# Optimization experiments

Hardware: AMD Instinct MI355X
Metric: run time of the kernel (lower is better)

## Reference

```python
import jax, jax.numpy as jnp
from jax import lax
import numpy as np

DN = ('NCHW', 'OIHW', 'NCHW')
DL = 64
B = 1024


def _cbr(x, w, g, b, stride, pad):
    """Conv2d(bias=False) -> BatchNorm2d (training stats, eps=1e-5) -> ReLU."""
    y = lax.conv_general_dilated(x, w, (stride, stride), [(pad, pad), (pad, pad)],
                                 dimension_numbers=DN)
    m = y.mean(axis=(0, 2, 3), keepdims=True)
    v = ((y - m) ** 2).mean(axis=(0, 2, 3), keepdims=True)  # biased var, as torch BN
    y = (y - m) * lax.rsqrt(v + 1e-5)
    return jax.nn.relu(y * g[None, :, None, None] + b[None, :, None, None])


def setup_inputs() -> dict:
    key = jax.random.key(0)
    ks = jax.random.split(key, 7)
    dl = DL
    inp = {
        'x': jax.random.normal(ks[0], (B, 3, 32, 32), jnp.float32),
        'w1': jax.random.normal(ks[1], (32, 3, 3, 3), jnp.float32) * 0.1,
        'w2': jax.random.normal(ks[2], (64, 32, 3, 3), jnp.float32) * 0.05,
        'w3': jax.random.normal(ks[3], (64, 64, 3, 3), jnp.float32) * 0.05,
        'wa': jax.random.normal(ks[4], (dl, 32, 1, 1), jnp.float32) * 0.1,
        'ws1': jax.random.normal(ks[5], (3 * dl, 32, 3, 3), jnp.float32) * 0.05,
        'ws2': jax.random.normal(ks[6], (3 * dl, 3 * dl, 3, 3), jnp.float32) * 0.03,
    }
    for i, c in enumerate([32, 64, 64, dl, 3 * dl, 3 * dl]):
        inp[f'g{i}'] = jnp.ones((c,), jnp.float32)
        inp[f'b{i}'] = jnp.zeros((c,), jnp.float32)
    return inp


def _encoder(x, w1, w2, w3, wa, ws1, ws2,
             g0, b0, g1, b1, g2, b2, g3, b3, g4, b4, g5, b5):
    dl = DL
    h = _cbr(x, w1, g0, b0, 1, 1)            # [B, 32, 32, 32]
    h = _cbr(h, w2, g1, b1, 1, 1)            # [B, 64, 32, 32]
    AS = _cbr(h, w3, g2, b2, 2, 1)           # [B, 64, 16, 16]
    A_, S_ = jnp.split(AS, 2, axis=1)        # each [B, 32, 16, 16]
    A = _cbr(A_, wa, g3, b3, 1, 0)           # [B, dl, 16, 16]
    S = _cbr(S_, ws1, g4, b4, 1, 1)          # [B, 3dl, 16, 16]
    S = _cbr(S, ws2, g5, b5, 2, 1)           # [B, 3dl, 8, 8]
    b, _, ps, _ = S.shape
    S = S.reshape(b, dl, 3, ps, ps)

    # per-sample conv_transpose2d(A[ii] [1,dl,pa,pa], weight S[ii] [dl,3,ps,ps],
    # stride=2, padding=3) expressed as lhs-dilated cross-correlation with
    # flipped, channel-swapped kernel; batched via vmap (no Python loop).
    pad = ps - 1 - 3  # k - 1 - torch_padding = 4

    def ct(a, s):  # a: [dl,16,16], s: [dl,3,8,8]
        wt = jnp.flip(s, (-2, -1)).transpose(1, 0, 2, 3)  # [3, dl, 8, 8]
        return lax.conv_general_dilated(a[None], wt, (1, 1),
                                        [(pad, pad), (pad, pad)],
                                        lhs_dilation=(2, 2),
                                        dimension_numbers=DN)[0]

    recon = jax.vmap(ct)(A, S)               # [B, 3, 32, 32]
    img = jax.nn.sigmoid(x)
    recon = jax.nn.sigmoid(recon)
    l1 = jnp.mean((img - recon) ** 2)
    l2 = jnp.mean(jax.nn.relu(S))
    logp = jax.nn.log_softmax(S, axis=1)     # softmax over dl axis (dim=1)
    l3 = -jnp.mean(jnp.exp(logp) * logp)
    return A, S, 0.1 * l1, 0.1 * l2, 0.1 * l3


def reference(x, w1, w2, w3, wa, ws1, ws2,
              g0, b0, g1, b1, g2, b2, g3, b3, g4, b4, g5, b5):
    return _encoder(x, w1, w2, w3, wa, ws1, ws2,
                    g0, b0, g1, b1, g2, b2, g3, b3, g4, b4, g5, b5)
```

## Files before the change

kernel.cpp:

```cpp
#include <hip/hip_runtime.h>
#include <math.h>


typedef __attribute__((ext_vector_type(8))) short short8v;
typedef __attribute__((ext_vector_type(4))) short short4v;
typedef __attribute__((ext_vector_type(4))) float f32x4;

__device__ __forceinline__ unsigned short f2bf(float f) {
  union { float f; unsigned u; } a; a.f = f;
  unsigned r = a.u + 0x7fffu + ((a.u >> 16) & 1u);
  return (unsigned short)(r >> 16);
}
__device__ __forceinline__ float bf2f(unsigned short h) {
  union { unsigned u; float f; } a; a.u = ((unsigned)h) << 16;
  return a.f;
}

__device__ __forceinline__ float wave_reduce(float v) {
#pragma unroll
  for (int off = 32; off; off >>= 1) v += __shfl_down(v, off, 64);
  return v;
}

template <int CI, int CO>
__device__ __forceinline__ void reord1(const float* __restrict__ w,
                                       unsigned short* __restrict__ wr,
                                       int idx) {
  int e = idx & 7;
  int t = idx >> 3;
  int co = t % CO; t /= CO;
  int ci8 = t % (CI / 8);
  int kk = t / (CI / 8);
  int ci = ci8 * 8 + e;
  wr[idx] = f2bf(w[((size_t)co * CI + ci) * 9 + kk]);
}

__global__ __launch_bounds__(256) void wreord_all_k(
    const float* __restrict__ w2, const float* __restrict__ w3,
    const float* __restrict__ ws1, const float* __restrict__ ws2,
    unsigned short* __restrict__ w2r, unsigned short* __restrict__ w3r,
    unsigned short* __restrict__ ws1r, unsigned short* __restrict__ ws2r) {
  int idx = blockIdx.x * 256 + threadIdx.x;
  if (idx < 18432) reord1<32, 64>(w2, w2r, idx);
  else if (idx < 55296) reord1<64, 64>(w3, w3r, idx - 18432);
  else if (idx < 110592) reord1<32, 192>(ws1, ws1r, idx - 55296);
  else if (idx < 442368) reord1<192, 192>(ws2, ws2r, idx - 110592);
}

__global__ __launch_bounds__(256) void conv0_k(const float* __restrict__ in,
                                               const float* __restrict__ w,
                                               unsigned short* __restrict__ outB,
                                               double* __restrict__ part) {
  __shared__ __align__(16) float tile[3][34][36];
  const int b = blockIdx.x;
  const int co0 = blockIdx.y * 8;
  const int tid = threadIdx.x;
  const int row = tid >> 3, x0 = (tid & 7) * 4;
  const int wv = tid >> 6;

  float* tf = &tile[0][0][0];
  for (int i = tid; i < 918; i += 256)
    *(float4*)(tf + i * 4) = make_float4(0.f, 0.f, 0.f, 0.f);
  __syncthreads();
  for (int i = tid; i < 768; i += 256) {
    int x4 = i & 7, yy = (i >> 3) & 31, c = i >> 8;
    float4 v = *(const float4*)&in[(((size_t)b * 3 + c) * 32 + yy) * 32 + x4 * 4];
    float* dst = &tile[c][yy + 1][1 + x4 * 4];
    dst[0] = v.x; dst[1] = v.y; dst[2] = v.z; dst[3] = v.w;
  }
  __syncthreads();

  float acc[4][8];
#pragma unroll
  for (int p = 0; p < 4; ++p)
#pragma unroll
    for (int co = 0; co < 8; ++co) acc[p][co] = 0.f;

#pragma unroll
  for (int c = 0; c < 3; ++c)
#pragma unroll
    for (int ky = 0; ky < 3; ++ky) {
      const float* tr = &tile[c][row + ky][x0];
      float4 vlo = *(const float4*)tr;
      float2 vhi = *(const float2*)(tr + 4);
      float v[6] = {vlo.x, vlo.y, vlo.z, vlo.w, vhi.x, vhi.y};
#pragma unroll
      for (int kx = 0; kx < 3; ++kx)
#pragma unroll
        for (int co = 0; co < 8; ++co) {
          float wvv = w[((size_t)(co0 + co) * 3 + c) * 9 + ky * 3 + kx];
#pragma unroll
          for (int p = 0; p < 4; ++p)
            acc[p][co] = fmaf(v[p + kx], wvv, acc[p][co]);
        }
    }
#pragma unroll
  for (int p = 0; p < 4; ++p) {
    short8v o;
#pragma unroll
    for (int co = 0; co < 8; ++co) o[co] = (short)f2bf(acc[p][co]);
    *(short8v*)&outB[(((size_t)b * 32 + row) * 32 + x0 + p) * 32 + co0] = o;
  }

  float s8[8], q8[8];
#pragma unroll
  for (int co = 0; co < 8; ++co) {
    float s = 0.f, q = 0.f;
#pragma unroll
    for (int p = 0; p < 4; ++p) {
      float v = acc[p][co];
      s += v;
      q = fmaf(v, v, q);
    }
    s8[co] = wave_reduce(s);
    q8[co] = wave_reduce(q);
  }
  __syncthreads();
  float* sb = (float*)tile;
  if ((tid & 63) == 0) {
#pragma unroll
    for (int co = 0; co < 8; ++co) {
      sb[wv * 8 + co] = s8[co];
      sb[32 + wv * 8 + co] = q8[co];
    }
  }
  __syncthreads();
  if (tid < 8) {
    float S = 0.f, Q = 0.f;
#pragma unroll
    for (int k = 0; k < 4; ++k) {
      S += sb[k * 8 + tid];
      Q += sb[32 + k * 8 + tid];
    }
    size_t slot = ((size_t)(co0 + tid) * 1024 + b) * 2;
    part[slot] = (double)S;
    part[slot + 1] = (double)Q;
  }
}

template <int CI_T, int CI0, int CI, int CIP, int CO, int COB, int IHW,
          int OHW, int STRIDE, int ORPB, int WM, int WN, int CTM, int CTN,
          bool OUT_BF16T>
__global__ __launch_bounds__(512) void convgemm_k(
    const unsigned short* __restrict__ inT, const float* __restrict__ ss,
    const unsigned short* __restrict__ wr_w, float* __restrict__ outF,
    unsigned short* __restrict__ outB, double* __restrict__ part) {
  constexpr int IR = (ORPB - 1) * STRIDE + 3;
  constexpr int IW2 = IHW + 2;
  constexpr int NPX = ORPB * OHW;
  constexpr int NPIX = OHW * OHW;
  constexpr bool SWZ = (STRIDE == 2);
  static_assert(WM * WN == 8, "8 waves");
  static_assert(WN * CTN * 16 == NPX, "px tiling");
  static_assert(WM * CTM * 16 == COB, "co tiling");
  static_assert((IR * IW2 * CIP) % 4 == 0, "zero fill");
  static_assert(IR * IW2 * CIP * 2 >= 8 * CTM * 16 * 2 * 4, "stats overlay");
  static_assert(!SWZ || (CI / 8) % 8 == 0, "swizzle octet closure");
  __shared__ __align__(16) unsigned short st[IR * IW2 * CIP];

  const int b = blockIdx.x;
  const int oy0 = blockIdx.y * ORPB;
  const int co_base = blockIdx.z * COB;
  const int tid = threadIdx.x;
  const int w = tid >> 6, l = tid & 63;
  const int l16 = l & 15, g = l >> 4;
  const int wrow = w / WN, wcol = w % WN;

  {
    uint2 z = make_uint2(0u, 0u);
    uint2* stz = (uint2*)st;
    constexpr int NZ = IR * IW2 * CIP / 4;
    for (int i = tid; i < NZ; i += 512) stz[i] = z;
  }
  __syncthreads();

  {
    constexpr int CPP = CI / 8;
    constexpr int NCH = IR * IHW * CPP;
    const int r0in = oy0 * STRIDE - 1;
    for (int i = tid; i < NCH; i += 512) {
      int c8 = i % CPP;
      int xx = (i / CPP) % IHW;
      int ir = i / (CPP * IHW);
      int iy = r0in + ir;
      if ((unsigned)iy < (unsigned)IHW) {
        short8v raw = *(const short8v*)&inT[(((size_t)b * IHW + iy) * IHW + xx) *
                                            CI_T + CI0 + c8 * 8];
        f32x4 sc0 = *(const f32x4*)&ss[CI0 + c8 * 8];
        f32x4 sc1 = *(const f32x4*)&ss[CI0 + c8 * 8 + 4];
        f32x4 sh0 = *(const f32x4*)&ss[CI_T + CI0 + c8 * 8];
        f32x4 sh1 = *(const f32x4*)&ss[CI_T + CI0 + c8 * 8 + 4];
        short4v lo, hi;
#pragma unroll
        for (int e = 0; e < 4; ++e) {
          float f = bf2f((unsigned short)raw[e]);
          f = fmaxf(fmaf(f, sc0[e], sh0[e]), 0.f);
          lo[e] = (short)f2bf(f);
        }
#pragma unroll
        for (int e = 0; e < 4; ++e) {
          float f = bf2f((unsigned short)raw[e + 4]);
          f = fmaxf(fmaf(f, sc1[e], sh1[e]), 0.f);
          hi[e] = (short)f2bf(f);
        }
        int xcol = xx + 1;
        int gran = SWZ ? (c8 ^ (xcol & 7)) : c8;
        int pp = SWZ ? ((xcol >> 1) & 1) : 0;
        unsigned short* dst = &st[(ir * IW2 + xcol) * CIP + gran * 8];
        *(short4v*)(dst + 4 * pp) = lo;
        *(short4v*)(dst + 4 * (1 - pp)) = hi;
      }
    }
  }
  __syncthreads();

  int prow[CTN], pxx[CTN];
#pragma unroll
  for (int pn = 0; pn < CTN; ++pn) {
    int pxl = (wcol * CTN + pn) * 16 + l16;
    int ly = pxl / OHW, lx = pxl % OHW;
    prow[pn] = (ly * STRIDE * IW2 + lx * STRIDE) * CIP;
    pxx[pn] = lx * STRIDE;
  }
  const int co_off = co_base + wrow * CTM * 16 + l16;

  f32x4 acc[CTM][CTN];
#pragma unroll
  for (int cm = 0; cm < CTM; ++cm)
#pragma unroll
    for (int pn = 0; pn < CTN; ++pn) {
      f32x4 z = {0.f, 0.f, 0.f, 0.f};
      acc[cm][pn] = z;
    }

#pragma unroll 3
  for (int kk = 0; kk < 9; ++kk) {
    const int ky = kk / 3, kx = kk % 3;
    const int rowadd = (ky * IW2 + kx) * CIP;
#pragma unroll
    for (int cs = 0; cs < CI / 32; ++cs) {
      short8v bfr[CTN];
#pragma unroll
      for (int pn = 0; pn < CTN; ++pn) {
        int col = pxx[pn] + kx;
        int gran = cs * 4 + g;
        int pp = 0;
        if (SWZ) {
          gran ^= (col & 7);
          pp = (col >> 1) & 1;
        }
        const unsigned short* bp = &st[prow[pn] + rowadd + gran * 8];
        short4v lo = *(const short4v*)(bp + 4 * pp);
        short4v hi = *(const short4v*)(bp + 4 * (1 - pp));
        short8v v = {lo[0], lo[1], lo[2], lo[3], hi[0], hi[1], hi[2], hi[3]};
        bfr[pn] = v;
      }
      const unsigned short* wb =
          wr_w + ((size_t)(kk * (CI / 8) + cs * 4 + g) * CO + co_off) * 8;
      short8v afr[CTM];
#pragma unroll
      for (int cm = 0; cm < CTM; ++cm)
        afr[cm] = *(const short8v*)(wb + cm * 128);
#pragma unroll
      for (int cm = 0; cm < CTM; ++cm)
#pragma unroll
        for (int pn = 0; pn < CTN; ++pn)
          acc[cm][pn] = __builtin_amdgcn_mfma_f32_16x16x32_bf16(
              afr[cm], bfr[pn], acc[cm][pn], 0, 0, 0);
    }
  }

#pragma unroll
  for (int cm = 0; cm < CTM; ++cm)
#pragma unroll
    for (int pn = 0; pn < CTN; ++pn) {
      int pxl = (wcol * CTN + pn) * 16 + l16;
      size_t pxg = (size_t)oy0 * OHW + pxl;
      int co = co_base + (wrow * CTM + cm) * 16 + g * 4;
      if (OUT_BF16T) {
        unsigned d0 = (unsigned)f2bf(acc[cm][pn][0]) |
                      ((unsigned)f2bf(acc[cm][pn][1]) << 16);
        unsigned d1 = (unsigned)f2bf(acc[cm][pn][2]) |
                      ((unsigned)f2bf(acc[cm][pn][3]) << 16);
        unsigned* dst = (unsigned*)&outB[((size_t)b * NPIX + pxg) * CO + co];
        dst[0] = d0;
        dst[1] = d1;
      } else {
#pragma unroll
        for (int r = 0; r < 4; ++r)
          outF[((size_t)b * CO + co + r) * NPIX + pxg] = acc[cm][pn][r];
      }
    }

  float sst[CTM][4], qst[CTM][4];
#pragma unroll
  for (int cm = 0; cm < CTM; ++cm)
#pragma unroll
    for (int r = 0; r < 4; ++r) {
      float s = 0.f, q = 0.f;
#pragma unroll
      for (int pn = 0; pn < CTN; ++pn) {
        float v = acc[cm][pn][r];
        s += v;
        q = fmaf(v, v, q);
      }
#pragma unroll
      for (int mask = 1; mask < 16; mask <<= 1) {
        s += __shfl_xor(s, mask, 64);
        q += __shfl_xor(q, mask, 64);
      }
      sst[cm][r] = s;
      qst[cm][r] = q;
    }
  __syncthreads();
  float* sbuf = (float*)st;
  float* qbuf = sbuf + 8 * CTM * 16;
  if (l16 == 0) {
#pragma unroll
    for (int cm = 0; cm < CTM; ++cm)
#pragma unroll
      for (int r = 0; r < 4; ++r) {
        sbuf[((w * CTM + cm) * 4 + g) * 4 + r] = sst[cm][r];
        qbuf[((w * CTM + cm) * 4 + g) * 4 + r] = qst[cm][r];
      }
  }
  __syncthreads();
  if (tid < COB) {
    int wrow_t = tid / (CTM * 16);
    int rem = tid % (CTM * 16);
    float S = 0.f, Q = 0.f;
#pragma unroll
    for (int j = 0; j < WN; ++j) {
      int wvx = wrow_t * WN + j;
      S += sbuf[(wvx * CTM) * 16 + rem];
      Q += qbuf[(wvx * CTM) * 16 + rem];
    }
    const int blk = blockIdx.x * gridDim.y + blockIdx.y;
    const int nblk = 1024 * gridDim.y;
    size_t slot = ((size_t)(co_base + tid) * nblk + blk) * 2;
    part[slot] = (double)S;
    part[slot + 1] = (double)Q;
  }
}

__global__ __launch_bounds__(256) void finalize_k(
    const double* __restrict__ part, int NB, const float* __restrict__ g,
    const float* __restrict__ bb, float* __restrict__ ss, int C, double invN) {
  __shared__ double sms[256], smq[256];
  const int c = blockIdx.x;
  const int t = threadIdx.x;
  double s = 0.0, q = 0.0;
  const double* base = part + (size_t)c * NB * 2;
  for (int i = t; i < NB; i += 256) {
    s += base[i * 2];
    q += base[i * 2 + 1];
  }
  sms[t] = s;
  smq[t] = q;
  __syncthreads();
  for (int st = 128; st; st >>= 1) {
    if (t < st) {
      sms[t] += sms[t + st];
      smq[t] += smq[t + st];
    }
    __syncthreads();
  }
  if (t == 0) {
    double mean = sms[0] * invN;
    double var = smq[0] * invN - mean * mean;
    float scale = g[c] * rsqrtf((float)var + 1e-5f);
    float shift = bb[c] - (float)mean * scale;
    ss[c] = scale;
    ss[C + c] = shift;
  }
}

__global__ __launch_bounds__(256) void conv1x1_k(
    const unsigned short* __restrict__ inT, const float* __restrict__ ss,
    const float* __restrict__ w, float* __restrict__ out,
    double* __restrict__ part) {
  __shared__ float sb1x[4][16], qb1x[4][16];
  const int b = blockIdx.x;
  const int co0 = blockIdx.y * 16;
  const int px = threadIdx.x;
  const int wv = threadIdx.x >> 6;
  float acc[16];
#pragma unroll
  for (int co = 0; co < 16; ++co) acc[co] = 0.f;
  const unsigned short* rowp = inT + ((size_t)b * 256 + px) * 64;
#pragma unroll
  for (int c8 = 0; c8 < 4; ++c8) {
    short8v raw = *(const short8v*)(rowp + c8 * 8);
#pragma unroll
    for (int e = 0; e < 8; ++e) {
      int c = c8 * 8 + e;
      float f = bf2f((unsigned short)raw[e]);
      f = fmaxf(fmaf(f, ss[c], ss[64 + c]), 0.f);
#pragma unroll
      for (int co = 0; co < 16; ++co)
        acc[co] = fmaf(f, w[(co0 + co) * 32 + c], acc[co]);
    }
  }
#pragma unroll
  for (int co = 0; co < 16; ++co)
    out[((size_t)b * 64 + co0 + co) * 256 + px] = acc[co];

#pragma unroll
  for (int co = 0; co < 16; ++co) {
    float s = wave_reduce(acc[co]);
    float q = wave_reduce(acc[co] * acc[co]);
    if ((threadIdx.x & 63) == 0) {
      sb1x[wv][co] = s;
      qb1x[wv][co] = q;
    }
  }
  __syncthreads();
  if (px < 16) {
    float S = 0.f, Q = 0.f;
#pragma unroll
    for (int k = 0; k < 4; ++k) {
      S += sb1x[k][px];
      Q += qb1x[k][px];
    }
    size_t slot = ((size_t)(co0 + px) * 1024 + b) * 2;
    part[slot] = (double)S;
    part[slot + 1] = (double)Q;
  }
}

__global__ __launch_bounds__(256) void convt_l1_k(float* __restrict__ A,
                                                  const float* __restrict__ S,
                                                  const float* __restrict__ x,
                                                  const float* __restrict__ ssA,
                                                  double* __restrict__ l1p) {
  __shared__ unsigned short Ab[8][256][8];
  __shared__ unsigned short Sb[4][16][3][72];
  __shared__ float sbred[4];
  const int b = blockIdx.x, tid = threadIdx.x;
  const int w = tid >> 6, l = tid & 63;
  const int g = l >> 4, c = l & 15;
  const int pa = w >> 1, pb = w & 1;

  float* Ag = A + (size_t)b * 16384;
  for (int dp = 0; dp < 32; ++dp) {
    int d = dp * 2;
    float f0 = Ag[(size_t)d * 256 + tid];
    float f1 = Ag[(size_t)(d + 1) * 256 + tid];
    f0 = fmaxf(fmaf(f0, ssA[d], ssA[64 + d]), 0.f);
    f1 = fmaxf(fmaf(f1, ssA[d + 1], ssA[64 + d + 1]), 0.f);
    Ag[(size_t)d * 256 + tid] = f0;
    Ag[(size_t)(d + 1) * 256 + tid] = f1;
    unsigned lo = f2bf(f0);
    unsigned hi = f2bf(f1);
    *(unsigned*)&Ab[d >> 3][tid][d & 7] = lo | (hi << 16);
  }
  const float* Sg = S + (size_t)b * 12288;
  for (int i = tid; i < 12288; i += 256) {
    int cch = i >> 6;
    int tap = i & 63;
    int d = cch / 3, t = cch - 3 * d;
    int ky = tap >> 3, kx = tap & 7;
    int par = (((ky & 1) ^ 1) << 1) | ((kx & 1) ^ 1);
    Sb[par][(ky >> 1) * 4 + (kx >> 1)][t][d] = f2bf(Sg[i]);
  }
  __syncthreads();

  f32x4 acc[16];
#pragma unroll
  for (int nt = 0; nt < 16; ++nt) {
    f32x4 z = {0.f, 0.f, 0.f, 0.f};
    acc[nt] = z;
  }

  const int shy = 1 + pa, shx = 1 + pb;
  for (int s = 0; s < 32; ++s) {
    const int tap = s >> 1;
    const int m = tap >> 2, n = tap & 3;
    const int dh = s & 1;
    short8v afr = {0, 0, 0, 0, 0, 0, 0, 0};
    if (c < 3) afr = *(const short8v*)&Sb[w][tap][c][dh * 32 + g * 8];
    const int ix = c + shx - n;
    const bool xok = (unsigned)ix < 16u;
    const int dblk = dh * 4 + g;
#pragma unroll
    for (int nt = 0; nt < 16; ++nt) {
      int iy = nt + shy - m;
      if ((unsigned)iy >= 16u) continue;
      short8v bfr = {0, 0, 0, 0, 0, 0, 0, 0};
      if (xok) bfr = *(const short8v*)&Ab[dblk][iy * 16 + ix][0];
      acc[nt] = __builtin_amdgcn_mfma_f32_16x16x32_bf16(afr, bfr, acc[nt],
                                                        0, 0, 0);
    }
  }

  float loc = 0.f;
  if (g == 0) {
    const float* xg = x + (size_t)b * 3072;
#pragma unroll
    for (int nt = 0; nt < 16; ++nt) {
      int oy = 2 * nt + pa, ox = 2 * c + pb;
#pragma unroll
      for (int r = 0; r < 3; ++r) {
        float recon = 1.f / (1.f + expf(-acc[nt][r]));
        float img = 1.f / (1.f + expf(-xg[r * 1024 + oy * 32 + ox]));
        float dd = img - recon;
        loc = fmaf(dd, dd, loc);
      }
    }
  }
  loc = wave_reduce(loc);
  if (l == 0) sbred[w] = loc;
  __syncthreads();
  if (tid == 0)
    l1p[b] = (double)(sbred[0] + sbred[1] + sbred[2] + sbred[3]);
}

__global__ __launch_bounds__(256) void loss23_k(float* __restrict__ S,
                                                const float* __restrict__ ss,
                                                double* __restrict__ l2p,
                                                double* __restrict__ l3p) {
  __shared__ float ssl[384];
  __shared__ float sb1[4], sb2[4];
  for (int i = threadIdx.x; i < 384; i += 256) ssl[i] = ss[i];
  __syncthreads();
  int gid = blockIdx.x * 256 + threadIdx.x;
  int b = gid / 192;
  int r = gid - b * 192;
  int t = r >> 6, p = r & 63;
  float* base = S + ((size_t)b * 192 + t) * 64 + p;
  float v[64];
  float l2 = 0.f, m = -1e30f;
#pragma unroll
  for (int d = 0; d < 64; ++d) {
    float raw = base[(size_t)d * 192];
    int cch = d * 3 + t;
    float f = fmaxf(fmaf(raw, ssl[cch], ssl[192 + cch]), 0.f);
    v[d] = f;
    m = fmaxf(m, f);
    l2 += f;
  }
#pragma unroll
  for (int d = 0; d < 64; ++d) base[(size_t)d * 192] = v[d];
  float Z = 0.f;
#pragma unroll
  for (int d = 0; d < 64; ++d) Z += expf(v[d] - m);
  float lZ = logf(Z);
  float l3 = 0.f;
#pragma unroll
  for (int d = 0; d < 64; ++d) {
    float lp = v[d] - m - lZ;
    l3 = fmaf(expf(lp), lp, l3);
  }
  l2 = wave_reduce(l2);
  l3 = wave_reduce(l3);
  int lane = threadIdx.x & 63, w = threadIdx.x >> 6;
  if (lane == 0) { sb1[w] = l2; sb2[w] = l3; }
  __syncthreads();
  if (threadIdx.x == 0) {
    l2p[blockIdx.x] = (double)(sb1[0] + sb1[1] + sb1[2] + sb1[3]);
    l3p[blockIdx.x] = (double)(sb2[0] + sb2[1] + sb2[2] + sb2[3]);
  }
}

__global__ __launch_bounds__(256) void scalars_k(const double* __restrict__ l1p,
                                                 const double* __restrict__ l2p,
                                                 const double* __restrict__ l3p,
                                                 float* __restrict__ out) {
  __shared__ double sm[256];
  const int t = threadIdx.x;

  double a = 0.0;
  for (int i = t; i < 1024; i += 256) a += l1p[i];
  sm[t] = a;
  __syncthreads();
  for (int s = 128; s; s >>= 1) {
    if (t < s) sm[t] += sm[t + s];
    __syncthreads();
  }
  double L1 = sm[0];
  __syncthreads();

  a = 0.0;
  for (int i = t; i < 768; i += 256) a += l2p[i];
  sm[t] = a;
  __syncthreads();
  for (int s = 128; s; s >>= 1) {
    if (t < s) sm[t] += sm[t + s];
    __syncthreads();
  }
  double L2 = sm[0];
  __syncthreads();

  a = 0.0;
  for (int i = t; i < 768; i += 256) a += l3p[i];
  sm[t] = a;
  __syncthreads();
  for (int s = 128; s; s >>= 1) {
    if (t < s) sm[t] += sm[t + s];
    __syncthreads();
  }
  double L3 = sm[0];

  if (t == 0) {
    out[0] = (float)(0.1 * L1 / 3145728.0);
    out[1] = (float)(0.1 * L2 / 12582912.0);
    out[2] = (float)(-0.1 * L3 / 12582912.0);
  }
}

extern "C" void kernel_launch(void* const* d_in, const int* in_sizes, int n_in,
                              void* d_out, int out_size, void* d_ws,
                              size_t ws_size, hipStream_t stream) {
  const float* x = (const float*)d_in[0];
  const float* w1 = (const float*)d_in[1];
  const float* w2 = (const float*)d_in[2];
  const float* w3 = (const float*)d_in[3];
  const float* wa = (const float*)d_in[4];
  const float* ws1 = (const float*)d_in[5];
  const float* ws2 = (const float*)d_in[6];
  const float* gb[12];
  for (int i = 0; i < 12; ++i) gb[i] = (const float*)d_in[7 + i];

  float* dout = (float*)d_out;
  float* Aout = dout;
  float* Sout = dout + 16777216LL;
  float* sc_out = dout + 29360128LL;

  float* wsf = (float*)d_ws;
  unsigned short* y1b = (unsigned short*)(wsf);
  unsigned short* y2b = (unsigned short*)(wsf + 16777216LL);
  unsigned short* y3b = (unsigned short*)(wsf + 50331648LL);
  unsigned short* y5b = (unsigned short*)(wsf + 58720256LL);
  unsigned short* wts = (unsigned short*)(wsf + 83886080LL);
  unsigned short* w2r = wts;
  unsigned short* w3r = wts + 18432;
  unsigned short* ws1r = wts + 55296;
  unsigned short* ws2r = wts + 110592;
  double* part = (double*)(wsf + 84107264LL);
  double* l1p = (double*)(wsf + 85680128LL);
  double* l2p = l1p + 1024;
  double* l3p = l2p + 768;
  float* ssL = (float*)(l3p + 768);
  float* ss0 = ssL, *ss1 = ssL + 384, *ss2 = ssL + 768;
  float* ss3 = ssL + 1152, *ss4 = ssL + 1536, *ss5 = ssL + 1920;

  wreord_all_k<<<1728, 256, 0, stream>>>(w2, w3, ws1, ws2, w2r, w3r, ws1r, ws2r);

  conv0_k<<<dim3(1024, 4), 256, 0, stream>>>(x, w1, y1b, part);
  finalize_k<<<32, 256, 0, stream>>>(part, 1024, gb[0], gb[1], ss0, 32, 1.0 / 1048576.0);

  convgemm_k<32, 0, 32, 36, 64, 64, 32, 32, 1, 8, 2, 4, 2, 4, true>
      <<<dim3(1024, 4, 1), 512, 0, stream>>>(y1b, ss0, w2r, nullptr, y2b, part);
  finalize_k<<<64, 256, 0, stream>>>(part, 4096, gb[2], gb[3], ss1, 64, 1.0 / 1048576.0);

  convgemm_k<64, 0, 64, 68, 64, 64, 32, 16, 2, 8, 2, 4, 2, 2, true>
      <<<dim3(1024, 2, 1), 512, 0, stream>>>(y2b, ss1, w3r, nullptr, y3b, part);
  finalize_k<<<64, 256, 0, stream>>>(part, 2048, gb[4], gb[5], ss2, 64, 1.0 / 262144.0);

  conv1x1_k<<<dim3(1024, 4), 256, 0, stream>>>(y3b, ss2, wa, Aout, part);
  finalize_k<<<64, 256, 0, stream>>>(part, 1024, gb[6], gb[7], ss3, 64, 1.0 / 262144.0);

  convgemm_k<64, 32, 32, 36, 192, 96, 16, 16, 1, 16, 2, 4, 3, 4, true>
      <<<dim3(1024, 1, 2), 512, 0, stream>>>(y3b, ss2, ws1r, nullptr, y5b, part);
  finalize_k<<<192, 256, 0, stream>>>(part, 1024, gb[8], gb[9], ss4, 192, 1.0 / 262144.0);

  convgemm_k<192, 0, 192, 196, 192, 192, 16, 8, 2, 4, 4, 2, 3, 1, false>
      <<<dim3(1024, 2, 1), 512, 0, stream>>>(y5b, ss4, ws2r, Sout, nullptr, part);
  finalize_k<<<192, 256, 0, stream>>>(part, 2048, gb[10], gb[11], ss5, 192, 1.0 / 65536.0);

  loss23_k<<<768, 256, 0, stream>>>(Sout, ss5, l2p, l3p);
  convt_l1_k<<<1024, 256, 0, stream>>>(Aout, Sout, x, ss3, l1p);
  scalars_k<<<1, 256, 0, stream>>>(l1p, l2p, l3p, sc_out);
}
```

Baseline: 676.4 us.

## Split conv input channels into LDS phases and fuse loss kernel into convt

The conv GEMM kernel now stages input channels in several phases, each with a smaller LDS tile, which should allow more resident blocks on the stride-2 layers. The separate loss2/loss3 kernel is removed, and its BN+ReLU, L2 sum and softmax entropy are computed inside the conv-transpose kernel. This avoids a second pass over S. The costs are extra barriers per phase and a softmax computed from bf16-rounded S values.

```diff
diff --git a/kernel.cpp b/kernel.cpp
--- a/kernel.cpp
+++ b/kernel.cpp
@@ -138,9 +138,9 @@
   }
 }
 
-template <int CI_T, int CI0, int CI, int CIP, int CO, int COB, int IHW,
-          int OHW, int STRIDE, int ORPB, int WM, int WN, int CTM, int CTN,
-          bool OUT_BF16T>
+template <int CI_T, int CI0, int CI, int NPH, int CIP, int CO, int COB,
+          int IHW, int OHW, int STRIDE, int ORPB, int WM, int WN, int CTM,
+          int CTN, bool OUT_BF16T>
 __global__ __launch_bounds__(512) void convgemm_k(
     const unsigned short* __restrict__ inT, const float* __restrict__ ss,
     const unsigned short* __restrict__ wr_w, float* __restrict__ outF,
@@ -149,13 +149,15 @@
   constexpr int IW2 = IHW + 2;
   constexpr int NPX = ORPB * OHW;
   constexpr int NPIX = OHW * OHW;
-  constexpr bool SWZ = (STRIDE == 2);
+  constexpr int CIS = CI / NPH;
+  constexpr int CPP = CIS / 8;
+  constexpr bool SWZ = (STRIDE == 2) && (CPP % 8 == 0);
+  static_assert(CI % NPH == 0 && CIS % 32 == 0, "phase split");
   static_assert(WM * WN == 8, "8 waves");
   static_assert(WN * CTN * 16 == NPX, "px tiling");
   static_assert(WM * CTM * 16 == COB, "co tiling");
   static_assert((IR * IW2 * CIP) % 4 == 0, "zero fill");
   static_assert(IR * IW2 * CIP * 2 >= 8 * CTM * 16 * 2 * 4, "stats overlay");
-  static_assert(!SWZ || (CI / 8) % 8 == 0, "swizzle octet closure");
   __shared__ __align__(16) unsigned short st[IR * IW2 * CIP];
 
   const int b = blockIdx.x;
@@ -172,47 +174,6 @@
     constexpr int NZ = IR * IW2 * CIP / 4;
     for (int i = tid; i < NZ; i += 512) stz[i] = z;
   }
-  __syncthreads();
-
-  {
-    constexpr int CPP = CI / 8;
-    constexpr int NCH = IR * IHW * CPP;
-    const int r0in = oy0 * STRIDE - 1;
-    for (int i = tid; i < NCH; i += 512) {
-      int c8 = i % CPP;
-      int xx = (i / CPP) % IHW;
-      int ir = i / (CPP * IHW);
-      int iy = r0in + ir;
-      if ((unsigned)iy < (unsigned)IHW) {
-        short8v raw = *(const short8v*)&inT[(((size_t)b * IHW + iy) * IHW + xx) *
-                                            CI_T + CI0 + c8 * 8];
-        f32x4 sc0 = *(const f32x4*)&ss[CI0 + c8 * 8];
-        f32x4 sc1 = *(const f32x4*)&ss[CI0 + c8 * 8 + 4];
-        f32x4 sh0 = *(const f32x4*)&ss[CI_T + CI0 + c8 * 8];
-        f32x4 sh1 = *(const f32x4*)&ss[CI_T + CI0 + c8 * 8 + 4];
-        short4v lo, hi;
-#pragma unroll
-        for (int e = 0; e < 4; ++e) {
-          float f = bf2f((unsigned short)raw[e]);
-          f = fmaxf(fmaf(f, sc0[e], sh0[e]), 0.f);
-          lo[e] = (short)f2bf(f);
-        }
-#pragma unroll
-        for (int e = 0; e < 4; ++e) {
-          float f = bf2f((unsigned short)raw[e + 4]);
-          f = fmaxf(fmaf(f, sc1[e], sh1[e]), 0.f);
-          hi[e] = (short)f2bf(f);
-        }
-        int xcol = xx + 1;
-        int gran = SWZ ? (c8 ^ (xcol & 7)) : c8;
-        int pp = SWZ ? ((xcol >> 1) & 1) : 0;
-        unsigned short* dst = &st[(ir * IW2 + xcol) * CIP + gran * 8];
-        *(short4v*)(dst + 4 * pp) = lo;
-        *(short4v*)(dst + 4 * (1 - pp)) = hi;
-      }
-    }
-  }
-  __syncthreads();
 
   int prow[CTN], pxx[CTN];
 #pragma unroll
@@ -233,40 +194,84 @@
       acc[cm][pn] = z;
     }
 
+  for (int ph = 0; ph < NPH; ++ph) {
+    __syncthreads();
+    {
+      const int CH0 = CI0 + ph * CIS;
+      constexpr int NCH = IR * IHW * CPP;
+      const int r0in = oy0 * STRIDE - 1;
+      for (int i = tid; i < NCH; i += 512) {
+        int c8 = i % CPP;
+        int xx = (i / CPP) % IHW;
+        int ir = i / (CPP * IHW);
+        int iy = r0in + ir;
+        if ((unsigned)iy < (unsigned)IHW) {
+          short8v raw = *(const short8v*)&inT[(((size_t)b * IHW + iy) * IHW +
+                                              xx) * CI_T + CH0 + c8 * 8];
+          f32x4 sc0 = *(const f32x4*)&ss[CH0 + c8 * 8];
+          f32x4 sc1 = *(const f32x4*)&ss[CH0 + c8 * 8 + 4];
+          f32x4 sh0 = *(const f32x4*)&ss[CI_T + CH0 + c8 * 8];
+          f32x4 sh1 = *(const f32x4*)&ss[CI_T + CH0 + c8 * 8 + 4];
+          short4v lo, hi;
+#pragma unroll
+          for (int e = 0; e < 4; ++e) {
+            float f = bf2f((unsigned short)raw[e]);
+            f = fmaxf(fmaf(f, sc0[e], sh0[e]), 0.f);
+            lo[e] = (short)f2bf(f);
+          }
+#pragma unroll
+          for (int e = 0; e < 4; ++e) {
+            float f = bf2f((unsigned short)raw[e + 4]);
+            f = fmaxf(fmaf(f, sc1[e], sh1[e]), 0.f);
+            hi[e] = (short)f2bf(f);
+          }
+          int xcol = xx + 1;
+          int gran = SWZ ? (c8 ^ (xcol & 7)) : c8;
+          int pp = SWZ ? ((xcol >> 1) & 1) : 0;
+          unsigned short* dst = &st[(ir * IW2 + xcol) * CIP + gran * 8];
+          *(short4v*)(dst + 4 * pp) = lo;
+          *(short4v*)(dst + 4 * (1 - pp)) = hi;
+        }
+      }
+    }
+    __syncthreads();
+
 #pragma unroll 3
-  for (int kk = 0; kk < 9; ++kk) {
-    const int ky = kk / 3, kx = kk % 3;
-    const int rowadd = (ky * IW2 + kx) * CIP;
-#pragma unroll
-    for (int cs = 0; cs < CI / 32; ++cs) {
-      short8v bfr[CTN];
-#pragma unroll
-      for (int pn = 0; pn < CTN; ++pn) {
-        int col = pxx[pn] + kx;
-        int gran = cs * 4 + g;
-        int pp = 0;
-        if (SWZ) {
-          gran ^= (col & 7);
-          pp = (col >> 1) & 1;
+    for (int kk = 0; kk < 9; ++kk) {
+      const int ky = kk / 3, kx = kk % 3;
+      const int rowadd = (ky * IW2 + kx) * CIP;
+#pragma unroll
+      for (int cs = 0; cs < CIS / 32; ++cs) {
+        short8v bfr[CTN];
+#pragma unroll
+        for (int pn = 0; pn < CTN; ++pn) {
+          int col = pxx[pn] + kx;
+          int gran = cs * 4 + g;
+          int pp = 0;
+          if (SWZ) {
+            gran ^= (col & 7);
+            pp = (col >> 1) & 1;
+          }
+          const unsigned short* bp = &st[prow[pn] + rowadd + gran * 8];
+          short4v lo = *(const short4v*)(bp + 4 * pp);
+          short4v hi = *(const short4v*)(bp + 4 * (1 - pp));
+          short8v v = {lo[0], lo[1], lo[2], lo[3], hi[0], hi[1], hi[2], hi[3]};
+          bfr[pn] = v;
         }
-        const unsigned short* bp = &st[prow[pn] + rowadd + gran * 8];
-        short4v lo = *(const short4v*)(bp + 4 * pp);
-        short4v hi = *(const short4v*)(bp + 4 * (1 - pp));
-        short8v v = {lo[0], lo[1], lo[2], lo[3], hi[0], hi[1], hi[2], hi[3]};
-        bfr[pn] = v;
-      }
-      const unsigned short* wb =
-          wr_w + ((size_t)(kk * (CI / 8) + cs * 4 + g) * CO + co_off) * 8;
-      short8v afr[CTM];
-#pragma unroll
-      for (int cm = 0; cm < CTM; ++cm)
-        afr[cm] = *(const short8v*)(wb + cm * 128);
-#pragma unroll
-      for (int cm = 0; cm < CTM; ++cm)
-#pragma unroll
-        for (int pn = 0; pn < CTN; ++pn)
-          acc[cm][pn] = __builtin_amdgcn_mfma_f32_16x16x32_bf16(
-              afr[cm], bfr[pn], acc[cm][pn], 0, 0, 0);
+        const unsigned short* wb =
+            wr_w + ((size_t)(kk * (CI / 8) + ph * CPP + cs * 4 + g) * CO +
+                    co_off) * 8;
+        short8v afr[CTM];
+#pragma unroll
+        for (int cm = 0; cm < CTM; ++cm)
+          afr[cm] = *(const short8v*)(wb + cm * 128);
+#pragma unroll
+        for (int cm = 0; cm < CTM; ++cm)
+#pragma unroll
+          for (int pn = 0; pn < CTN; ++pn)
+            acc[cm][pn] = __builtin_amdgcn_mfma_f32_16x16x32_bf16(
+                afr[cm], bfr[pn], acc[cm][pn], 0, 0, 0);
+      }
     }
   }
 
@@ -428,14 +433,14 @@
   }
 }
 
-__global__ __launch_bounds__(256) void convt_l1_k(float* __restrict__ A,
-                                                  const float* __restrict__ S,
-                                                  const float* __restrict__ x,
-                                                  const float* __restrict__ ssA,
-                                                  double* __restrict__ l1p) {
+__global__ __launch_bounds__(256) void convt_l1_k(
+    float* __restrict__ A, float* __restrict__ S, const float* __restrict__ x,
+    const float* __restrict__ ssA, const float* __restrict__ ssS,
+    double* __restrict__ l1p, double* __restrict__ l2p,
+    double* __restrict__ l3p) {
   __shared__ unsigned short Ab[8][256][8];
   __shared__ unsigned short Sb[4][16][3][72];
-  __shared__ float sbred[4];
+  __shared__ float sbred[4], sbl2[4], sbl3[4];
   const int b = blockIdx.x, tid = threadIdx.x;
   const int w = tid >> 6, l = tid & 63;
   const int g = l >> 4, c = l & 15;
@@ -454,16 +459,52 @@
     unsigned hi = f2bf(f1);
     *(unsigned*)&Ab[d >> 3][tid][d & 7] = lo | (hi << 16);
   }
-  const float* Sg = S + (size_t)b * 12288;
+
+  float* Sg = S + (size_t)b * 12288;
+  float l2loc = 0.f;
   for (int i = tid; i < 12288; i += 256) {
+    float raw = Sg[i];
     int cch = i >> 6;
+    float f = fmaxf(fmaf(raw, ssS[cch], ssS[192 + cch]), 0.f);
+    Sg[i] = f;
+    l2loc += f;
     int tap = i & 63;
     int d = cch / 3, t = cch - 3 * d;
     int ky = tap >> 3, kx = tap & 7;
     int par = (((ky & 1) ^ 1) << 1) | ((kx & 1) ^ 1);
-    Sb[par][(ky >> 1) * 4 + (kx >> 1)][t][d] = f2bf(Sg[i]);
-  }
-  __syncthreads();
+    Sb[par][(ky >> 1) * 4 + (kx >> 1)][t][d] = f2bf(f);
+  }
+  __syncthreads();
+
+  float l3loc = 0.f;
+  if (tid < 192) {
+    int par = tid / 48, rr = tid - par * 48;
+    int tap = rr / 3, t = rr - tap * 3;
+    const unsigned short* rowp = &Sb[par][tap][t][0];
+    short8v rv[8];
+#pragma unroll
+    for (int k = 0; k < 8; ++k) rv[k] = *(const short8v*)(rowp + k * 8);
+    float m = -1e30f;
+#pragma unroll
+    for (int k = 0; k < 8; ++k)
+#pragma unroll
+      for (int e = 0; e < 8; ++e)
+        m = fmaxf(m, bf2f((unsigned short)rv[k][e]));
+    float Z = 0.f;
+#pragma unroll
+    for (int k = 0; k < 8; ++k)
+#pragma unroll
+      for (int e = 0; e < 8; ++e)
+        Z += expf(bf2f((unsigned short)rv[k][e]) - m);
+    float lZ = logf(Z);
+#pragma unroll
+    for (int k = 0; k < 8; ++k)
+#pragma unroll
+      for (int e = 0; e < 8; ++e) {
+        float lp = bf2f((unsigned short)rv[k][e]) - m - lZ;
+        l3loc = fmaf(expf(lp), lp, l3loc);
+      }
+  }
 
   f32x4 acc[16];
 #pragma unroll
@@ -509,56 +550,14 @@
     }
   }
   loc = wave_reduce(loc);
-  if (l == 0) sbred[w] = loc;
-  __syncthreads();
-  if (tid == 0)
+  l2loc = wave_reduce(l2loc);
+  l3loc = wave_reduce(l3loc);
+  if (l == 0) { sbred[w] = loc; sbl2[w] = l2loc; sbl3[w] = l3loc; }
+  __syncthreads();
+  if (tid == 0) {
     l1p[b] = (double)(sbred[0] + sbred[1] + sbred[2] + sbred[3]);
-}
-
-__global__ __launch_bounds__(256) void loss23_k(float* __restrict__ S,
-                                                const float* __restrict__ ss,
-                                                double* __restrict__ l2p,
-                                                double* __restrict__ l3p) {
-  __shared__ float ssl[384];
-  __shared__ float sb1[4], sb2[4];
-  for (int i = threadIdx.x; i < 384; i += 256) ssl[i] = ss[i];
-  __syncthreads();
-  int gid = blockIdx.x * 256 + threadIdx.x;
-  int b = gid / 192;
-  int r = gid - b * 192;
-  int t = r >> 6, p = r & 63;
-  float* base = S + ((size_t)b * 192 + t) * 64 + p;
-  float v[64];
-  float l2 = 0.f, m = -1e30f;
-#pragma unroll
-  for (int d = 0; d < 64; ++d) {
-    float raw = base[(size_t)d * 192];
-    int cch = d * 3 + t;
-    float f = fmaxf(fmaf(raw, ssl[cch], ssl[192 + cch]), 0.f);
-    v[d] = f;
-    m = fmaxf(m, f);
-    l2 += f;
-  }
-#pragma unroll
-  for (int d = 0; d < 64; ++d) base[(size_t)d * 192] = v[d];
-  float Z = 0.f;
-#pragma unroll
-  for (int d = 0; d < 64; ++d) Z += expf(v[d] - m);
-  float lZ = logf(Z);
-  float l3 = 0.f;
-#pragma unroll
-  for (int d = 0; d < 64; ++d) {
-    float lp = v[d] - m - lZ;
-    l3 = fmaf(expf(lp), lp, l3);
-  }
-  l2 = wave_reduce(l2);
-  l3 = wave_reduce(l3);
-  int lane = threadIdx.x & 63, w = threadIdx.x >> 6;
-  if (lane == 0) { sb1[w] = l2; sb2[w] = l3; }
-  __syncthreads();
-  if (threadIdx.x == 0) {
-    l2p[blockIdx.x] = (double)(sb1[0] + sb1[1] + sb1[2] + sb1[3]);
-    l3p[blockIdx.x] = (double)(sb2[0] + sb2[1] + sb2[2] + sb2[3]);
+    l2p[b] = (double)(sbl2[0] + sbl2[1] + sbl2[2] + sbl2[3]);
+    l3p[b] = (double)(sbl3[0] + sbl3[1] + sbl3[2] + sbl3[3]);
   }
 }
 
@@ -581,7 +580,7 @@
   __syncthreads();
 
   a = 0.0;
-  for (int i = t; i < 768; i += 256) a += l2p[i];
+  for (int i = t; i < 1024; i += 256) a += l2p[i];
   sm[t] = a;
   __syncthreads();
   for (int s = 128; s; s >>= 1) {
@@ -592,7 +591,7 @@
   __syncthreads();
 
   a = 0.0;
-  for (int i = t; i < 768; i += 256) a += l3p[i];
+  for (int i = t; i < 1024; i += 256) a += l3p[i];
   sm[t] = a;
   __syncthreads();
   for (int s = 128; s; s >>= 1) {
@@ -639,8 +638,8 @@
   double* part = (double*)(wsf + 84107264LL);
   double* l1p = (double*)(wsf + 85680128LL);
   double* l2p = l1p + 1024;
-  double* l3p = l2p + 768;
-  float* ssL = (float*)(l3p + 768);
+  double* l3p = l2p + 1024;
+  float* ssL = (float*)(l3p + 1024);
   float* ss0 = ssL, *ss1 = ssL + 384, *ss2 = ssL + 768;
   float* ss3 = ssL + 1152, *ss4 = ssL + 1536, *ss5 = ssL + 1920;
 
@@ -649,26 +648,25 @@
   conv0_k<<<dim3(1024, 4), 256, 0, stream>>>(x, w1, y1b, part);
   finalize_k<<<32, 256, 0, stream>>>(part, 1024, gb[0], gb[1], ss0, 32, 1.0 / 1048576.0);
 
-  convgemm_k<32, 0, 32, 36, 64, 64, 32, 32, 1, 8, 2, 4, 2, 4, true>
+  convgemm_k<32, 0, 32, 1, 36, 64, 64, 32, 32, 1, 8, 2, 4, 2, 4, true>
       <<<dim3(1024, 4, 1), 512, 0, stream>>>(y1b, ss0, w2r, nullptr, y2b, part);
   finalize_k<<<64, 256, 0, stream>>>(part, 4096, gb[2], gb[3], ss1, 64, 1.0 / 1048576.0);
 
-  convgemm_k<64, 0, 64, 68, 64, 64, 32, 16, 2, 8, 2, 4, 2, 2, true>
+  convgemm_k<64, 0, 64, 2, 36, 64, 64, 32, 16, 2, 8, 2, 4, 2, 2, true>
       <<<dim3(1024, 2, 1), 512, 0, stream>>>(y2b, ss1, w3r, nullptr, y3b, part);
   finalize_k<<<64, 256, 0, stream>>>(part, 2048, gb[4], gb[5], ss2, 64, 1.0 / 262144.0);
 
   conv1x1_k<<<dim3(1024, 4), 256, 0, stream>>>(y3b, ss2, wa, Aout, part);
   finalize_k<<<64, 256, 0, stream>>>(part, 1024, gb[6], gb[7], ss3, 64, 1.0 / 262144.0);
 
-  convgemm_k<64, 32, 32, 36, 192, 96, 16, 16, 1, 16, 2, 4, 3, 4, true>
+  convgemm_k<64, 32, 32, 1, 36, 192, 96, 16, 16, 1, 16, 2, 4, 3, 4, true>
       <<<dim3(1024, 1, 2), 512, 0, stream>>>(y3b, ss2, ws1r, nullptr, y5b, part);
   finalize_k<<<192, 256, 0, stream>>>(part, 1024, gb[8], gb[9], ss4, 192, 1.0 / 262144.0);
 
-  convgemm_k<192, 0, 192, 196, 192, 192, 16, 8, 2, 4, 4, 2, 3, 1, false>
+  convgemm_k<192, 0, 192, 3, 68, 192, 192, 16, 8, 2, 4, 4, 2, 3, 1, false>
       <<<dim3(1024, 2, 1), 512, 0, stream>>>(y5b, ss4, ws2r, Sout, nullptr, part);
   finalize_k<<<192, 256, 0, stream>>>(part, 2048, gb[10], gb[11], ss5, 192, 1.0 / 65536.0);
 
-  loss23_k<<<768, 256, 0, stream>>>(Sout, ss5, l2p, l3p);
-  convt_l1_k<<<1024, 256, 0, stream>>>(Aout, Sout, x, ss3, l1p);
+  convt_l1_k<<<1024, 256, 0, stream>>>(Aout, Sout, x, ss3, ss5, l1p, l2p, l3p);
   scalars_k<<<1, 256, 0, stream>>>(l1p, l2p, l3p, sc_out);
 }
```

New measurement: 659.6 us, median of 5. 1.03x faster.
